# Kernel optimization log

Measured on AMD Instinct MI355X. Metric: run time of the kernel, lower is better.

Reference implementation:

```python
import jax, jax.numpy as jnp
import numpy as np
from jax.scipy.linalg import solve_triangular
from jax.scipy.special import logsumexp

N, T, M, K = 16384, 60, 8, 2


def setup_inputs() -> dict:
    key = jax.random.key(0)
    k1, k2, k3, k4 = jax.random.split(key, 4)
    mu = jax.random.normal(k1, (N, T, M, K), dtype=jnp.float32)
    # Build SPD covariance: sigma = A A^T + 0.5 I (module runs cholesky on it)
    A = 0.3 * jax.random.normal(k2, (N, T, M, K, K), dtype=jnp.float32)
    sigma = A @ jnp.swapaxes(A, -1, -2) + 0.5 * jnp.eye(K, dtype=jnp.float32)
    pi = jax.random.normal(k3, (N, M), dtype=jnp.float32)
    x = jax.random.normal(k4, (N, T, K), dtype=jnp.float32)
    mask = jnp.ones((N, T), dtype=jnp.float32)
    return {"mu": mu, "sigma": sigma, "pi": pi, "x": x, "mask": mask}


def reference(mu, sigma, pi, x, mask):
    k = mu.shape[-1]
    LOG_2PI = 1.8378770664093453
    # batched small-matrix Cholesky: (N,T,m,k,k)
    L = jnp.linalg.cholesky(sigma)
    diff = x[:, :, None, :] - mu                       # (N,T,m,k)
    # triangular solve L z = diff -> Mahalanobis term
    z = solve_triangular(L, diff[..., None], lower=True)[..., 0]
    maha = jnp.sum(z * z, axis=-1)                     # (N,T,m)
    log_det = jnp.sum(jnp.log(jnp.diagonal(L, axis1=-2, axis2=-1)), axis=-1)
    mvn_lp = -0.5 * (k * LOG_2PI + maha) - log_det     # (N,T,m)
    # Categorical(logits=pi) -> normalized log-probs, broadcast over T
    log_pi = jax.nn.log_softmax(pi, axis=-1)[:, None, :]  # (N,1,m)
    gmm_lp = logsumexp(log_pi + mvn_lp, axis=-1)       # (N,T)
    comp_loss = -gmm_lp
    # mask_reduce_losses: per-timestep mean over valid batch entries, then sum
    n_pred = jnp.sum(mask, axis=0)                     # (T,)
    t_losses = jnp.sum(comp_loss * mask, axis=0) / n_pred
    return jnp.sum(t_losses)
```

## Files before the change

kernel.cpp:

```cpp
#include <hip/hip_runtime.h>

#define T_DIM 60
#define NBLK 3840

typedef float v4f __attribute__((ext_vector_type(4)));
typedef float v2f __attribute__((ext_vector_type(2)));

__global__ __launch_bounds__(256)
void loss_fused_kernel(const float* __restrict__ mu,
                       const float* __restrict__ sigma,
                       const float* __restrict__ pi,
                       const float* __restrict__ x,
                       const float* __restrict__ mask,
                       float* __restrict__ loss_p,
                       float* __restrict__ mask_p) {
    __shared__ float bl[T_DIM], bm[T_DIM];
    __shared__ float s_lsepi[8];
    const float LOG_2PI = 1.8378770664093453f;
    int tid = threadIdx.x;
    int E0 = blockIdx.x * 256;
    int n_base = E0 / T_DIM;
    int ncnt = (E0 + 255) / T_DIM - n_base + 1;

    if (tid < T_DIM) { bl[tid] = 0.0f; bm[tid] = 0.0f; }
    if (tid < ncnt) {
        const float* pr = pi + (size_t)(n_base + tid) * 8;
        float q0 = pr[0], q1 = pr[1], q2 = pr[2], q3 = pr[3];
        float q4 = pr[4], q5 = pr[5], q6 = pr[6], q7 = pr[7];
        float mx = fmaxf(fmaxf(fmaxf(q0, q1), fmaxf(q2, q3)),
                         fmaxf(fmaxf(q4, q5), fmaxf(q6, q7)));
        float s = __expf(q0 - mx) + __expf(q1 - mx) + __expf(q2 - mx) +
                  __expf(q3 - mx) + __expf(q4 - mx) + __expf(q5 - mx) +
                  __expf(q6 - mx) + __expf(q7 - mx);
        s_lsepi[tid] = mx + __logf(s);
    }
    __syncthreads();

    int l = tid & 7;
    int oct = tid >> 3;
    int e = E0 + oct;
    int n = e / T_DIM;
    int t = e - n * T_DIM;
    int nb = n - n_base;

#pragma unroll
    for (int it = 0; it < 8; ++it) {
        v4f sg = __builtin_nontemporal_load((const v4f*)sigma + (size_t)e * 8 + l);
        v2f m2 = __builtin_nontemporal_load((const v2f*)mu + (size_t)e * 8 + l);
        v2f xv = __builtin_nontemporal_load((const v2f*)x + e);
        float mk = __builtin_nontemporal_load(mask + e);
        float p  = pi[(size_t)n * 8 + l];

        float a = sg.x, b = sg.y, c = sg.w;
        float d1 = xv.x - m2.x, d2 = xv.y - m2.y;
        float det = a * c - b * b;
        float maha = (c * d1 * d1 - 2.0f * b * d1 * d2 + a * d2 * d2) / det;
        float lp = p - LOG_2PI - 0.5f * (maha + __logf(det));

        float s = __expf(lp);
        s += __shfl_xor(s, 1);
        s += __shfl_xor(s, 2);
        s += __shfl_xor(s, 4);

        if (l == 0) {
            float v = (s_lsepi[nb] - __logf(s)) * mk;
            atomicAdd(&bl[t], v);
            atomicAdd(&bm[t], mk);
        }

        e += 32;
        t += 32;
        if (t >= T_DIM) { t -= T_DIM; n += 1; nb += 1; }
    }
    __syncthreads();
    if (tid < T_DIM) {
        loss_p[(size_t)tid * NBLK + blockIdx.x] = bl[tid];
        mask_p[(size_t)tid * NBLK + blockIdx.x] = bm[tid];
    }
}

__global__ void reduce_t_kernel(const float* __restrict__ loss_p,
                                const float* __restrict__ mask_p,
                                float* __restrict__ tvals, int nblocks) {
    int t = blockIdx.x;
    const float* lrow = loss_p + (size_t)t * nblocks;
    const float* mrow = mask_p + (size_t)t * nblocks;
    float sl = 0.0f, sm = 0.0f;
    for (int i = threadIdx.x; i < nblocks; i += blockDim.x) {
        sl += lrow[i]; sm += mrow[i];
    }
#pragma unroll
    for (int off = 32; off > 0; off >>= 1) {
        sl += __shfl_down(sl, off); sm += __shfl_down(sm, off);
    }
    __shared__ float wl[4], wm[4];
    int lane = threadIdx.x & 63, w = threadIdx.x >> 6;
    if (lane == 0) { wl[w] = sl; wm[w] = sm; }
    __syncthreads();
    if (threadIdx.x == 0)
        tvals[t] = (wl[0] + wl[1] + wl[2] + wl[3]) /
                   (wm[0] + wm[1] + wm[2] + wm[3]);
}

__global__ void final_sum_kernel(const float* __restrict__ tvals,
                                 float* __restrict__ out) {
    int tid = threadIdx.x;
    float s = (tid < T_DIM) ? tvals[tid] : 0.0f;
#pragma unroll
    for (int off = 32; off > 0; off >>= 1)
        s += __shfl_down(s, off);
    if (tid == 0) out[0] = s;
}

extern "C" void kernel_launch(void* const* d_in, const int* in_sizes, int n_in,
                              void* d_out, int out_size, void* d_ws, size_t ws_size,
                              hipStream_t stream) {
    const float* mu    = (const float*)d_in[0];
    const float* sigma = (const float*)d_in[1];
    const float* pi    = (const float*)d_in[2];
    const float* x     = (const float*)d_in[3];
    const float* mask  = (const float*)d_in[4];
    float* out = (float*)d_out;
    float* ws = (float*)d_ws;
    float* loss_p = ws;
    float* mask_p = ws + (size_t)T_DIM * NBLK;
    float* tvals  = ws + (size_t)2 * T_DIM * NBLK;

    hipLaunchKernelGGL(loss_fused_kernel, dim3(NBLK), dim3(256), 0, stream,
                       mu, sigma, pi, x, mask, loss_p, mask_p);
    hipLaunchKernelGGL(reduce_t_kernel, dim3(T_DIM), dim3(256), 0, stream,
                       loss_p, mask_p, tvals, NBLK);
    hipLaunchKernelGGL(final_sum_kernel, dim3(1), dim3(64), 0, stream,
                       tvals, out);
}
```

Before: 231.2 us.

## Stage x, mask and pi in LDS, use rcp, and fold final sum into atomics

Each block now loads x, mask and pi once into shared memory, so the unrolled loop no longer issues redundant global loads for them. The division by the determinant becomes a hardware reciprocal, and the LOG_2PI constant is folded into the staged pi values. The separate final-sum kernel is removed: out is zeroed in the first kernel and each reduce block atomically adds its per-timestep value, saving one launch. The risks are nondeterministic float atomic ordering, slightly lower reciprocal precision, and more LDS use per block.

```diff
diff --git a/kernel.cpp b/kernel.cpp
--- a/kernel.cpp
+++ b/kernel.cpp
@@ -13,9 +13,13 @@
                        const float* __restrict__ x,
                        const float* __restrict__ mask,
                        float* __restrict__ loss_p,
-                       float* __restrict__ mask_p) {
+                       float* __restrict__ mask_p,
+                       float* __restrict__ out) {
     __shared__ float bl[T_DIM], bm[T_DIM];
     __shared__ float s_lsepi[8];
+    __shared__ float s_piv[48];
+    __shared__ v2f   s_x[256];
+    __shared__ float s_mk[256];
     const float LOG_2PI = 1.8378770664093453f;
     int tid = threadIdx.x;
     int E0 = blockIdx.x * 256;
@@ -23,8 +27,14 @@
     int ncnt = (E0 + 255) / T_DIM - n_base + 1;
 
     if (tid < T_DIM) { bl[tid] = 0.0f; bm[tid] = 0.0f; }
+    s_x[tid]  = __builtin_nontemporal_load((const v2f*)x + E0 + tid);
+    s_mk[tid] = __builtin_nontemporal_load(mask + E0 + tid);
+    if (tid < 8 * ncnt)
+        s_piv[tid] = pi[(size_t)n_base * 8 + tid] - LOG_2PI;
+    if (blockIdx.x == 0 && tid == 0) out[0] = 0.0f;
+    __syncthreads();
     if (tid < ncnt) {
-        const float* pr = pi + (size_t)(n_base + tid) * 8;
+        const float* pr = s_piv + tid * 8;
         float q0 = pr[0], q1 = pr[1], q2 = pr[2], q3 = pr[3];
         float q4 = pr[4], q5 = pr[5], q6 = pr[6], q7 = pr[7];
         float mx = fmaxf(fmaxf(fmaxf(q0, q1), fmaxf(q2, q3)),
@@ -32,30 +42,32 @@
         float s = __expf(q0 - mx) + __expf(q1 - mx) + __expf(q2 - mx) +
                   __expf(q3 - mx) + __expf(q4 - mx) + __expf(q5 - mx) +
                   __expf(q6 - mx) + __expf(q7 - mx);
-        s_lsepi[tid] = mx + __logf(s);
+        s_lsepi[tid] = mx + __logf(s) + LOG_2PI;
     }
     __syncthreads();
 
     int l = tid & 7;
     int oct = tid >> 3;
-    int e = E0 + oct;
-    int n = e / T_DIM;
-    int t = e - n * T_DIM;
-    int nb = n - n_base;
+    int idx = oct;
+    size_t e = (size_t)E0 + oct;
+    int n0 = (E0 + oct) / T_DIM;
+    int t = (E0 + oct) - n0 * T_DIM;
+    int nb = n0 - n_base;
 
 #pragma unroll
     for (int it = 0; it < 8; ++it) {
-        v4f sg = __builtin_nontemporal_load((const v4f*)sigma + (size_t)e * 8 + l);
-        v2f m2 = __builtin_nontemporal_load((const v2f*)mu + (size_t)e * 8 + l);
-        v2f xv = __builtin_nontemporal_load((const v2f*)x + e);
-        float mk = __builtin_nontemporal_load(mask + e);
-        float p  = pi[(size_t)n * 8 + l];
+        v4f sg = __builtin_nontemporal_load((const v4f*)sigma + e * 8 + l);
+        v2f m2 = __builtin_nontemporal_load((const v2f*)mu + e * 8 + l);
+        v2f xv = s_x[idx];
+        float mk = s_mk[idx];
+        float pv = s_piv[nb * 8 + l];
 
         float a = sg.x, b = sg.y, c = sg.w;
         float d1 = xv.x - m2.x, d2 = xv.y - m2.y;
         float det = a * c - b * b;
-        float maha = (c * d1 * d1 - 2.0f * b * d1 * d2 + a * d2 * d2) / det;
-        float lp = p - LOG_2PI - 0.5f * (maha + __logf(det));
+        float rdet = __builtin_amdgcn_rcpf(det);
+        float maha = (c * d1 * d1 - 2.0f * b * d1 * d2 + a * d2 * d2) * rdet;
+        float lp = pv - 0.5f * (maha + __logf(det));
 
         float s = __expf(lp);
         s += __shfl_xor(s, 1);
@@ -69,8 +81,9 @@
         }
 
         e += 32;
+        idx += 32;
         t += 32;
-        if (t >= T_DIM) { t -= T_DIM; n += 1; nb += 1; }
+        if (t >= T_DIM) { t -= T_DIM; nb += 1; }
     }
     __syncthreads();
     if (tid < T_DIM) {
@@ -81,7 +94,7 @@
 
 __global__ void reduce_t_kernel(const float* __restrict__ loss_p,
                                 const float* __restrict__ mask_p,
-                                float* __restrict__ tvals, int nblocks) {
+                                float* __restrict__ out, int nblocks) {
     int t = blockIdx.x;
     const float* lrow = loss_p + (size_t)t * nblocks;
     const float* mrow = mask_p + (size_t)t * nblocks;
@@ -98,18 +111,8 @@
     if (lane == 0) { wl[w] = sl; wm[w] = sm; }
     __syncthreads();
     if (threadIdx.x == 0)
-        tvals[t] = (wl[0] + wl[1] + wl[2] + wl[3]) /
-                   (wm[0] + wm[1] + wm[2] + wm[3]);
-}
-
-__global__ void final_sum_kernel(const float* __restrict__ tvals,
-                                 float* __restrict__ out) {
-    int tid = threadIdx.x;
-    float s = (tid < T_DIM) ? tvals[tid] : 0.0f;
-#pragma unroll
-    for (int off = 32; off > 0; off >>= 1)
-        s += __shfl_down(s, off);
-    if (tid == 0) out[0] = s;
+        atomicAdd(out, (wl[0] + wl[1] + wl[2] + wl[3]) /
+                       (wm[0] + wm[1] + wm[2] + wm[3]));
 }
 
 extern "C" void kernel_launch(void* const* d_in, const int* in_sizes, int n_in,
@@ -124,12 +127,9 @@
     float* ws = (float*)d_ws;
     float* loss_p = ws;
     float* mask_p = ws + (size_t)T_DIM * NBLK;
-    float* tvals  = ws + (size_t)2 * T_DIM * NBLK;
 
     hipLaunchKernelGGL(loss_fused_kernel, dim3(NBLK), dim3(256), 0, stream,
-                       mu, sigma, pi, x, mask, loss_p, mask_p);
+                       mu, sigma, pi, x, mask, loss_p, mask_p, out);
     hipLaunchKernelGGL(reduce_t_kernel, dim3(T_DIM), dim3(256), 0, stream,
-                       loss_p, mask_p, tvals, NBLK);
-    hipLaunchKernelGGL(final_sum_kernel, dim3(1), dim3(64), 0, stream,
-                       tvals, out);
+                       loss_p, mask_p, out, NBLK);
 }
```

After: 228.3 us. Within noise of the previous version (-1.3%).
